# Kernel tuning notes

Hardware: AMD Instinct MI355X
Metric: run time of the kernel (lower is better)

Reference implementation:

```python
import jax, jax.numpy as jnp
import numpy as np

N, T, F_IN, F_OUT, E = 20000, 4, 64, 64, 640000


def setup_inputs() -> dict:
    key = jax.random.key(0)
    k1, k2, k3, k4, k5, k6 = jax.random.split(key, 6)
    node_features = jax.random.normal(k1, (N, T, F_IN), dtype=jnp.float32)
    edge_weights = jax.random.uniform(k2, (T, E), dtype=jnp.float32)
    src = jax.random.randint(k3, (E,), 0, N, dtype=jnp.int32)
    dst = jax.random.randint(k4, (E,), 0, N, dtype=jnp.int32)
    W = jax.random.normal(k5, (F_OUT, F_IN), dtype=jnp.float32) / np.sqrt(F_IN)
    b = jax.random.normal(k6, (F_OUT,), dtype=jnp.float32) * 0.01
    return {"node_features": node_features, "edge_weights": edge_weights,
            "src": src, "dst": dst, "W": W, "b": b}


def reference(node_features, edge_weights, src, dst, W, b):
    # u_mul_e: gather source node features and scale by per-edge, per-time weight
    # edge_weights (T, E) -> transposed (E, T) -> broadcast over feature dim
    msg = node_features[src] * edge_weights.T[:, :, None]          # (E, T, F_IN)
    # fn.sum: scatter-sum messages into destination nodes
    h = jax.ops.segment_sum(msg, dst, num_segments=node_features.shape[0])  # (N, T, F_IN)
    # nn.Linear(in_features, out_features)
    return h @ W.T + b                                             # (N, T, F_OUT)
```

## Files before the change

### kernel.cpp

```cpp
#include <hip/hip_runtime.h>

#define N_NODES 20000
#define T_STEPS 4
#define F_DIM   64
#define E_EDGES 640000
#define ROWS    (N_NODES * T_STEPS)
#define ROW_ELEMS (T_STEPS * F_DIM)

#define RB       64
#define NRANGE   313
#define CAPF     3072
#define PART_BLOCKS   256
#define EPB      2500
#define TRANSFORM_BLOCKS (ROWS / 64)
#define OVF_CAP  4096

__device__ __forceinline__ unsigned short f32_to_bf16_rne(float f) {
    unsigned u = __float_as_uint(f);
    u += 0x7FFFu + ((u >> 16) & 1u);
    return (unsigned short)(u >> 16);
}
__device__ __forceinline__ float bf16_to_f32(unsigned short h) {
    return __uint_as_float((unsigned)h << 16);
}
__device__ __forceinline__ unsigned w_to_u10(float f) {
    unsigned q = __float2uint_rn(f * 1024.0f);
    return q > 1023u ? 1023u : q;
}

__device__ __forceinline__ float dec_w(uint2 r, int t) {
    const unsigned q = t == 0 ? (r.x >> 16) & 1023u
                     : t == 1 ? (((r.x >> 26) & 63u) | ((r.y & 15u) << 6))
                     : t == 2 ? (r.y >> 4) & 1023u
                     :          (r.y >> 14) & 1023u;
    return (float)q * (1.0f / 1024.0f);
}

__global__ __launch_bounds__(256) void build_kernel(
    const float* __restrict__ x, const float* __restrict__ W,
    unsigned short* __restrict__ yb,
    const int* __restrict__ src, const int* __restrict__ dst,
    const float* __restrict__ ew,
    int* __restrict__ gcnt, uint2* __restrict__ bkt,
    int4* __restrict__ ovf, int* __restrict__ ovf_cnt)
{
    __shared__ uint2 rec8[EPB];
    __shared__ unsigned short rid[EPB];
    __shared__ int off[NRANGE + 1];
    __shared__ int cur[NRANGE];
    __shared__ int gb[NRANGE];
    __shared__ int s[256];

    const int tid = threadIdx.x;

    if (blockIdx.x < PART_BLOCKS) {
        int* hcnt = gb;
        for (int i = tid; i < NRANGE; i += 256) hcnt[i] = 0;
        __syncthreads();
        const int base = blockIdx.x * EPB;

        for (int j = 0; j < 10; ++j) {
            const int idx = j * 256 + tid;
            if (idx < EPB) atomicAdd(&hcnt[dst[base + idx] >> 6], 1);
        }
        __syncthreads();

        int c0 = 0, c1 = 0;
        if (2 * tid < NRANGE)     c0 = hcnt[2 * tid];
        if (2 * tid + 1 < NRANGE) c1 = hcnt[2 * tid + 1];
        const int p = c0 + c1;
        s[tid] = p;
        __syncthreads();
        for (int o = 1; o < 256; o <<= 1) {
            const int v = (tid >= o) ? s[tid - o] : 0;
            __syncthreads();
            s[tid] += v;
            __syncthreads();
        }
        const int excl = s[tid] - p;
        if (2 * tid < NRANGE) { off[2 * tid] = excl; cur[2 * tid] = excl; }
        if (2 * tid + 1 <= NRANGE) {
            off[2 * tid + 1] = excl + c0;
            if (2 * tid + 1 < NRANGE) cur[2 * tid + 1] = excl + c0;
        }
        __syncthreads();

        for (int j = 0; j < 10; ++j) {
            const int idx = j * 256 + tid;
            if (idx < EPB) {
                const int e = base + idx;
                const unsigned w0 = w_to_u10(ew[e]);
                const unsigned w1 = w_to_u10(ew[E_EDGES + e]);
                const unsigned w2 = w_to_u10(ew[2 * E_EDGES + e]);
                const unsigned w3 = w_to_u10(ew[3 * E_EDGES + e]);
                const unsigned ss = (unsigned)src[e];
                const int d = dst[e];
                const unsigned lo = ss | (w0 << 16) | ((w1 & 63u) << 26);
                const unsigned hi = (w1 >> 6) | (w2 << 4) | (w3 << 14) |
                                    ((unsigned)(d & 63) << 24);
                const int r = d >> 6;
                const int pth = atomicAdd(&cur[r], 1);
                rec8[pth] = make_uint2(lo, hi);
                rid[pth]  = (unsigned short)r;
            }
        }
        __syncthreads();

        for (int r = tid; r < NRANGE; r += 256)
            gb[r] = atomicAdd(&gcnt[r], cur[r] - off[r]);
        __syncthreads();

        for (int i = tid; i < EPB; i += 256) {
            const int r = (int)rid[i];
            const int slot = gb[r] + (i - off[r]);
            const uint2 rc = rec8[i];
            if (slot < CAPF) {
                bkt[(size_t)r * CAPF + slot] = rc;
            } else {
                const int o = atomicAdd(ovf_cnt, 1);
                if (o < OVF_CAP) {
                    int4 q; q.x = (int)rc.x; q.y = (int)rc.y;
                    q.z = r * RB + (int)((rc.y >> 24) & 63u); q.w = 0;
                    ovf[o] = q;
                }
            }
        }
        return;
    }

    float* wt = (float*)rec8;
    const int row0 = (blockIdx.x - PART_BLOCKS) * 64;

    {
        const int o  = tid & 63;
        const int fb = (tid >> 6) * 16;
#pragma unroll
        for (int k = 0; k < 16; ++k) {
            const int f = fb + k;
            wt[f * 64 + o] = W[o * 64 + f];
        }
    }
    __syncthreads();

    const int rg = tid >> 4;
    const int oq = (tid & 15) * 4;

    float acc[4][4];
#pragma unroll
    for (int i = 0; i < 4; ++i)
#pragma unroll
        for (int j = 0; j < 4; ++j) acc[i][j] = 0.0f;

    const float4* xg4 = (const float4*)(x + (size_t)(row0 + rg * 4) * 64);

#pragma unroll 4
    for (int fc = 0; fc < 16; ++fc) {
        float4 xv[4];
#pragma unroll
        for (int i = 0; i < 4; ++i) xv[i] = xg4[i * 16 + fc];
#pragma unroll
        for (int j = 0; j < 4; ++j) {
            const int f = fc * 4 + j;
            const float4 w4 = *(const float4*)&wt[f * 64 + oq];
            const float xj0 = j == 0 ? xv[0].x : j == 1 ? xv[0].y : j == 2 ? xv[0].z : xv[0].w;
            const float xj1 = j == 0 ? xv[1].x : j == 1 ? xv[1].y : j == 2 ? xv[1].z : xv[1].w;
            const float xj2 = j == 0 ? xv[2].x : j == 1 ? xv[2].y : j == 2 ? xv[2].z : xv[2].w;
            const float xj3 = j == 0 ? xv[3].x : j == 1 ? xv[3].y : j == 2 ? xv[3].z : xv[3].w;
            acc[0][0] += xj0 * w4.x; acc[0][1] += xj0 * w4.y; acc[0][2] += xj0 * w4.z; acc[0][3] += xj0 * w4.w;
            acc[1][0] += xj1 * w4.x; acc[1][1] += xj1 * w4.y; acc[1][2] += xj1 * w4.z; acc[1][3] += xj1 * w4.w;
            acc[2][0] += xj2 * w4.x; acc[2][1] += xj2 * w4.y; acc[2][2] += xj2 * w4.z; acc[2][3] += xj2 * w4.w;
            acc[3][0] += xj3 * w4.x; acc[3][1] += xj3 * w4.y; acc[3][2] += xj3 * w4.z; acc[3][3] += xj3 * w4.w;
        }
    }

#pragma unroll
    for (int i = 0; i < 4; ++i) {
        const int r = row0 + rg * 4 + i;
        ushort4 h;
        h.x = f32_to_bf16_rne(acc[i][0]);
        h.y = f32_to_bf16_rne(acc[i][1]);
        h.z = f32_to_bf16_rne(acc[i][2]);
        h.w = f32_to_bf16_rne(acc[i][3]);
        *(ushort4*)(yb + (size_t)r * 64 + oq) = h;
    }
}

__global__ __launch_bounds__(256) void sort_kernel(
    const int* __restrict__ gcnt, uint2* __restrict__ bkt,
    unsigned int* __restrict__ nodeinfo)
{
    __shared__ uint2 lrec[CAPF];
    __shared__ int h2[RB], ps[RB], c2[RB];
    const int tid = threadIdx.x;
    const int r   = blockIdx.x;

    int m = gcnt[r]; if (m > CAPF) m = CAPF;
    uint2* rowp = bkt + (size_t)r * CAPF;

    for (int i = tid; i < m; i += 256) lrec[i] = rowp[i];
    if (tid < RB) { h2[tid] = 0; c2[tid] = 0; }
    __syncthreads();

    for (int i = tid; i < m; i += 256) atomicAdd(&h2[(lrec[i].y >> 24) & 63u], 1);
    __syncthreads();

    if (tid == 0) {
        int run = 0;
        for (int i = 0; i < RB; ++i) { ps[i] = run; run += h2[i]; }
    }
    __syncthreads();

    if (tid < RB)
        nodeinfo[r * RB + tid] = (unsigned)ps[tid] | ((unsigned)h2[tid] << 16);

    for (int i = tid; i < m; i += 256) {
        const uint2 rc = lrec[i];
        const int d6 = (rc.y >> 24) & 63;
        const int rk = atomicAdd(&c2[d6], 1);
        rowp[ps[d6] + rk] = rc;
    }
}

#define BATCH4(RP, K0)                                                        \
    {                                                                         \
        const uint2 R0 = (RP)[(K0) + 0], R1 = (RP)[(K0) + 1],                 \
                    R2 = (RP)[(K0) + 2], R3 = (RP)[(K0) + 3];                 \
        const ushort4 V0 = *(const ushort4*)(yb + (size_t)(R0.x & 0xFFFFu) * ROW_ELEMS + l4); \
        const ushort4 V1 = *(const ushort4*)(yb + (size_t)(R1.x & 0xFFFFu) * ROW_ELEMS + l4); \
        const ushort4 V2 = *(const ushort4*)(yb + (size_t)(R2.x & 0xFFFFu) * ROW_ELEMS + l4); \
        const ushort4 V3 = *(const ushort4*)(yb + (size_t)(R3.x & 0xFFFFu) * ROW_ELEMS + l4); \
        float w;                                                              \
        w = dec_w(R0, t);                                                     \
        acc.x += bf16_to_f32(V0.x) * w; acc.y += bf16_to_f32(V0.y) * w;       \
        acc.z += bf16_to_f32(V0.z) * w; acc.w += bf16_to_f32(V0.w) * w;       \
        w = dec_w(R1, t);                                                     \
        acc.x += bf16_to_f32(V1.x) * w; acc.y += bf16_to_f32(V1.y) * w;       \
        acc.z += bf16_to_f32(V1.z) * w; acc.w += bf16_to_f32(V1.w) * w;       \
        w = dec_w(R2, t);                                                     \
        acc.x += bf16_to_f32(V2.x) * w; acc.y += bf16_to_f32(V2.y) * w;       \
        acc.z += bf16_to_f32(V2.z) * w; acc.w += bf16_to_f32(V2.w) * w;       \
        w = dec_w(R3, t);                                                     \
        acc.x += bf16_to_f32(V3.x) * w; acc.y += bf16_to_f32(V3.y) * w;       \
        acc.z += bf16_to_f32(V3.z) * w; acc.w += bf16_to_f32(V3.w) * w;       \
    }

__global__ __launch_bounds__(256) void accumulate_kernel(
    const unsigned short* __restrict__ yb, const uint2* __restrict__ bkt,
    const unsigned int* __restrict__ nodeinfo,
    const int4* __restrict__ ovf, const int* __restrict__ ovf_cnt,
    const float* __restrict__ b, float* __restrict__ out)
{
    const int lane = threadIdx.x & 63;
    const int n    = blockIdx.x * 4 + (threadIdx.x >> 6);
    const int t    = lane >> 4;
    const int l4   = lane * 4;

    const unsigned info = nodeinfo[n];
    const int r = n >> 6;
    const uint2* rp = bkt + (size_t)r * CAPF + (info & 0xFFFFu);
    const int d = (int)(info >> 16);

    float4 acc = make_float4(0.f, 0.f, 0.f, 0.f);

    int k = 0;
    for (; k + 8 <= d; k += 8) { BATCH4(rp, k); BATCH4(rp, k + 4); }
    if (k + 4 <= d) { BATCH4(rp, k); k += 4; }
    for (; k < d; ++k) {
        const uint2 rr = rp[k];
        const float w = dec_w(rr, t);
        const ushort4 v = *(const ushort4*)(yb + (size_t)(rr.x & 0xFFFFu) * ROW_ELEMS + l4);
        acc.x += bf16_to_f32(v.x) * w;
        acc.y += bf16_to_f32(v.y) * w;
        acc.z += bf16_to_f32(v.z) * w;
        acc.w += bf16_to_f32(v.w) * w;
    }

    {
        int m = *ovf_cnt;
        if (m > OVF_CAP) m = OVF_CAP;
        for (int i = 0; i < m; ++i) {
            const int4 rr = ovf[i];
            if (rr.z == n) {
                const uint2 r2 = make_uint2((unsigned)rr.x, (unsigned)rr.y);
                const float w = dec_w(r2, t);
                const ushort4 v = *(const ushort4*)(yb + (size_t)(r2.x & 0xFFFFu) * ROW_ELEMS + l4);
                acc.x += bf16_to_f32(v.x) * w;
                acc.y += bf16_to_f32(v.y) * w;
                acc.z += bf16_to_f32(v.z) * w;
                acc.w += bf16_to_f32(v.w) * w;
            }
        }
    }

    const float4 bv = *(const float4*)(b + (lane & 15) * 4);
    acc.x += bv.x; acc.y += bv.y; acc.z += bv.z; acc.w += bv.w;
    *(float4*)(out + (size_t)n * ROW_ELEMS + l4) = acc;
}

extern "C" void kernel_launch(void* const* d_in, const int* in_sizes, int n_in,
                              void* d_out, int out_size, void* d_ws, size_t ws_size,
                              hipStream_t stream) {
    const float* x   = (const float*)d_in[0];
    const float* ew  = (const float*)d_in[1];
    const int*   src = (const int*)  d_in[2];
    const int*   dst = (const int*)  d_in[3];
    const float* W   = (const float*)d_in[4];
    const float* b   = (const float*)d_in[5];
    float*       out = (float*)d_out;

    char* ws = (char*)d_ws;
    size_t off = 0;
    auto alloc = [&](size_t bytes) {
        void* p = ws + off;
        off += (bytes + 255) & ~(size_t)255;
        return p;
    };
    unsigned short* yb       = (unsigned short*)alloc((size_t)ROWS * 64 * 2);
    int*            gcnt     = (int*)  alloc((NRANGE + 1) * sizeof(int));
    int4*           ovf      = (int4*) alloc((size_t)OVF_CAP * sizeof(int4));
    unsigned int*   nodeinfo = (unsigned int*)alloc((size_t)NRANGE * RB * 4);
    uint2*          bkt      = (uint2*)alloc((size_t)NRANGE * CAPF * sizeof(uint2));
    int*            ovf_cnt  = gcnt + NRANGE;
    (void)ws_size;

    hipError_t err = hipMemsetAsync(gcnt, 0, (NRANGE + 1) * sizeof(int), stream);
    (void)err;
    build_kernel<<<PART_BLOCKS + TRANSFORM_BLOCKS, 256, 0, stream>>>(
        x, W, yb, src, dst, ew, gcnt, bkt, ovf, ovf_cnt);
    sort_kernel<<<NRANGE, 256, 0, stream>>>(gcnt, bkt, nodeinfo);
    accumulate_kernel<<<N_NODES / 4, 256, 0, stream>>>(
        yb, bkt, nodeinfo, ovf, ovf_cnt, b, out);
}
```

Before: 156.4 us.

## Use 512-thread build blocks; fuse histogram with record packing in registers

The build kernel now launches 512 threads per block. In the partition path, each thread loads and packs its edges once, keeps them in registers and builds the histogram in the same pass, then runs a single-level 512-wide scan. This removes the separate histogram pass that re-read dst. The transform path now covers 128 rows per block, halving the block count. The hidden transform code must match the new 128-row mapping, and the larger blocks raise per-thread register pressure and may lower occupancy.

Result: no change. 154.9 us (median of 2 runs) (-1.0%).

```diff
diff --git a/kernel.cpp b/kernel.cpp
--- a/kernel.cpp
+++ b/kernel.cpp
@@ -12,7 +12,7 @@
 #define CAPF     3072
 #define PART_BLOCKS   256
 #define EPB      2500
-#define TRANSFORM_BLOCKS (ROWS / 64)
+#define TRANSFORM_BLOCKS (ROWS / 128)
 #define OVF_CAP  4096
 
 __device__ __forceinline__ unsigned short f32_to_bf16_rne(float f) {
@@ -36,7 +36,7 @@
     return (float)q * (1.0f / 1024.0f);
 }
 
-__global__ __launch_bounds__(256) void build_kernel(
+__global__ __launch_bounds__(512) void build_kernel(
     const float* __restrict__ x, const float* __restrict__ W,
     unsigned short* __restrict__ yb,
     const int* __restrict__ src, const int* __restrict__ dst,
@@ -46,47 +46,25 @@
 {
     __shared__ uint2 rec8[EPB];
     __shared__ unsigned short rid[EPB];
-    __shared__ int off[NRANGE + 1];
+    __shared__ int off[NRANGE];
     __shared__ int cur[NRANGE];
     __shared__ int gb[NRANGE];
-    __shared__ int s[256];
+    __shared__ int s[512];
 
     const int tid = threadIdx.x;
 
     if (blockIdx.x < PART_BLOCKS) {
         int* hcnt = gb;
-        for (int i = tid; i < NRANGE; i += 256) hcnt[i] = 0;
+        for (int i = tid; i < NRANGE; i += 512) hcnt[i] = 0;
         __syncthreads();
         const int base = blockIdx.x * EPB;
 
-        for (int j = 0; j < 10; ++j) {
-            const int idx = j * 256 + tid;
-            if (idx < EPB) atomicAdd(&hcnt[dst[base + idx] >> 6], 1);
-        }
-        __syncthreads();
-
-        int c0 = 0, c1 = 0;
-        if (2 * tid < NRANGE)     c0 = hcnt[2 * tid];
-        if (2 * tid + 1 < NRANGE) c1 = hcnt[2 * tid + 1];
-        const int p = c0 + c1;
-        s[tid] = p;
-        __syncthreads();
-        for (int o = 1; o < 256; o <<= 1) {
-            const int v = (tid >= o) ? s[tid - o] : 0;
-            __syncthreads();
-            s[tid] += v;
-            __syncthreads();
-        }
-        const int excl = s[tid] - p;
-        if (2 * tid < NRANGE) { off[2 * tid] = excl; cur[2 * tid] = excl; }
-        if (2 * tid + 1 <= NRANGE) {
-            off[2 * tid + 1] = excl + c0;
-            if (2 * tid + 1 < NRANGE) cur[2 * tid + 1] = excl + c0;
-        }
-        __syncthreads();
-
-        for (int j = 0; j < 10; ++j) {
-            const int idx = j * 256 + tid;
+        unsigned lo5[5], hi5[5];
+        int r5[5];
+#pragma unroll
+        for (int j = 0; j < 5; ++j) {
+            const int idx = j * 512 + tid;
+            r5[j] = -1;
             if (idx < EPB) {
                 const int e = base + idx;
                 const unsigned w0 = w_to_u10(ew[e]);
@@ -95,22 +73,46 @@
                 const unsigned w3 = w_to_u10(ew[3 * E_EDGES + e]);
                 const unsigned ss = (unsigned)src[e];
                 const int d = dst[e];
-                const unsigned lo = ss | (w0 << 16) | ((w1 & 63u) << 26);
-                const unsigned hi = (w1 >> 6) | (w2 << 4) | (w3 << 14) |
-                                    ((unsigned)(d & 63) << 24);
-                const int r = d >> 6;
-                const int pth = atomicAdd(&cur[r], 1);
-                rec8[pth] = make_uint2(lo, hi);
-                rid[pth]  = (unsigned short)r;
+                lo5[j] = ss | (w0 << 16) | ((w1 & 63u) << 26);
+                hi5[j] = (w1 >> 6) | (w2 << 4) | (w3 << 14) |
+                         ((unsigned)(d & 63) << 24);
+                r5[j] = d >> 6;
+                atomicAdd(&hcnt[r5[j]], 1);
             }
         }
         __syncthreads();
 
-        for (int r = tid; r < NRANGE; r += 256)
-            gb[r] = atomicAdd(&gcnt[r], cur[r] - off[r]);
-        __syncthreads();
-
-        for (int i = tid; i < EPB; i += 256) {
+        const int p = (tid < NRANGE) ? hcnt[tid] : 0;
+        s[tid] = p;
+        __syncthreads();
+        for (int o = 1; o < 512; o <<= 1) {
+            const int v = (tid >= o) ? s[tid - o] : 0;
+            __syncthreads();
+            s[tid] += v;
+            __syncthreads();
+        }
+        if (tid < NRANGE) {
+            const int excl = s[tid] - p;
+            off[tid] = excl;
+            cur[tid] = excl;
+        }
+        __syncthreads();
+
+#pragma unroll
+        for (int j = 0; j < 5; ++j) {
+            if (r5[j] >= 0) {
+                const int pth = atomicAdd(&cur[r5[j]], 1);
+                rec8[pth] = make_uint2(lo5[j], hi5[j]);
+                rid[pth]  = (unsigned short)r5[j];
+            }
+        }
+        __syncthreads();
+
+        if (tid < NRANGE)
+            gb[tid] = atomicAdd(&gcnt[tid], cur[tid] - off[tid]);
+        __syncthreads();
+
+        for (int i = tid; i < EPB; i += 512) {
             const int r = (int)rid[i];
             const int slot = gb[r] + (i - off[r]);
             const uint2 rc = rec8[i];
@@ -129,13 +131,13 @@
     }
 
     float* wt = (float*)rec8;
-    const int row0 = (blockIdx.x - PART_BLOCKS) * 64;
+    const int row0 = (blockIdx.x - PART_BLOCKS) * 128;
 
     {
         const int o  = tid & 63;
-        const int fb = (tid >> 6) * 16;
-#pragma unroll
-        for (int k = 0; k < 16; ++k) {
+        const int fb = (tid >> 6) * 8;
+#pragma unroll
+        for (int k = 0; k < 8; ++k) {
             const int f = fb + k;
             wt[f * 64 + o] = W[o * 64 + f];
         }
@@ -325,7 +327,7 @@
 
     hipError_t err = hipMemsetAsync(gcnt, 0, (NRANGE + 1) * sizeof(int), stream);
     (void)err;
-    build_kernel<<<PART_BLOCKS + TRANSFORM_BLOCKS, 256, 0, stream>>>(
+    build_kernel<<<PART_BLOCKS + TRANSFORM_BLOCKS, 512, 0, stream>>>(
         x, W, yb, src, dst, ew, gcnt, bkt, ovf, ovf_cnt);
     sort_kernel<<<NRANGE, 256, 0, stream>>>(gcnt, bkt, nodeinfo);
     accumulate_kernel<<<N_NODES / 4, 256, 0, stream>>>(
```
